# Kernel tuning notes

Hardware: AMD Instinct MI355X
Metric: run time of the kernel (lower is better)

Reference implementation:

```python
import jax, jax.numpy as jnp
import numpy as np

NUM_HEADS = 16
EMBED_DIM = 1024
HEAD_DIM = EMBED_DIM // NUM_HEADS  # 64


def setup_inputs() -> dict:
    key = jax.random.key(0)
    k1, k2, k3 = jax.random.split(key, 3)
    x = jax.random.normal(k1, (2, 2048, EMBED_DIM), dtype=jnp.float32)
    # torch Linear(head_dim, 3*head_dim): weight [3*hd, hd], bias [3*hd]
    # stored here as W_qkv [hd, 3*hd] so that y = x @ W_qkv + b
    lim = 1.0 / np.sqrt(HEAD_DIM)
    W_qkv = jax.random.uniform(k2, (HEAD_DIM, 3 * HEAD_DIM), minval=-lim, maxval=lim, dtype=jnp.float32)
    b_qkv = jax.random.uniform(k3, (3 * HEAD_DIM,), minval=-lim, maxval=lim, dtype=jnp.float32)
    return {"x": x, "W_qkv": W_qkv, "b_qkv": b_qkv}


def reference(x, W_qkv, b_qkv):
    B, T, E = x.shape
    # [B, T, E] -> [B, H, T, hd]
    xh = x.reshape(B, T, NUM_HEADS, HEAD_DIM).transpose(0, 2, 1, 3)
    qkv = xh @ W_qkv + b_qkv  # [B, H, T, 3*hd], shared weights across heads
    q, k, v = jnp.split(qkv, 3, axis=-1)
    scale = 1.0 / jnp.sqrt(jnp.asarray(HEAD_DIM, dtype=x.dtype))
    scores = jnp.einsum('bhqd,bhkd->bhqk', q, k) * scale  # [B, H, T, T]
    attn = jax.nn.softmax(scores, axis=-1)
    out = jnp.einsum('bhqk,bhkd->bhqd', attn, v)  # [B, H, T, hd]
    return out.transpose(0, 2, 1, 3).reshape(B, T, E)
```

## Files before the change

kernel.cpp:

```cpp
#include <hip/hip_runtime.h>
#include <hip/hip_bf16.h>

#define T_SEQ   2048
#define EMBED   1024
#define HD      64
#define NHEADS  16
#define NBH     32
#define QSCALE  0.18033688011112042f

typedef __attribute__((ext_vector_type(8))) short short8;
typedef __attribute__((ext_vector_type(4))) float f32x4;
typedef __attribute__((ext_vector_type(2))) unsigned int uint2v;

#if __has_builtin(__builtin_amdgcn_exp2f)
#define EXP2F __builtin_amdgcn_exp2f
#else
#define EXP2F exp2f
#endif

__device__ __forceinline__ ushort bf16r(float f) {
  union { float f; unsigned u; } v; v.f = f;
  return (ushort)((v.u + 0x8000u) >> 16);
}

__device__ __forceinline__ unsigned pk2bf(float a, float b) {
  union { float f; unsigned u; } ua, ub; ua.f = a; ub.f = b;
  return __builtin_amdgcn_perm(ub.u + 0x8000u, ua.u + 0x8000u, 0x07060302u);
}

__device__ __forceinline__ void async16(const ushort* g, ushort* l) {
  __builtin_amdgcn_global_load_lds(
      (const __attribute__((address_space(1))) unsigned int*)g,
      (__attribute__((address_space(3))) unsigned int*)l, 16, 0, 0);
}

__global__ __launch_bounds__(256) void prep_w(const float* __restrict__ W,
                                              ushort* __restrict__ Wg) {
  const int i = blockIdx.x * 256 + threadIdx.x;
  const int d = i / 192, c = i - d * 192;
  const int phys = c * 64 + (((d >> 3) ^ (c & 7)) << 3) + (d & 7);
  Wg[phys] = bf16r(W[i]);
}

__global__ __launch_bounds__(256) void qkv_proj(
    const float* __restrict__ x, const ushort* __restrict__ Wg,
    const float* __restrict__ bias,
    ushort* __restrict__ Qws, ushort* __restrict__ Kws,
    ushort* __restrict__ Vtws) {
  __shared__ ushort WtL[192 * 64];
  __shared__ float bl[192];

  const int bx = blockIdx.x;
  const int b  = bx >> 9;
  const int h  = (bx >> 5) & 15;
  const int t0 = (bx & 31) * 64;
  const int tid = threadIdx.x;
  const int wave = tid >> 6, lane = tid & 63;
  const int quad = lane >> 4, n16 = lane & 15;

  const int trow = t0 + wave * 16 + n16;
  const float* xr = x + ((size_t)(b * T_SEQ + trow)) * EMBED + h * HD;
  short8 xa[2];
#pragma unroll
  for (int ks = 0; ks < 2; ks++) {
    f32x4 v0 = *(const f32x4*)(xr + ks * 32 + quad * 8);
    f32x4 v1 = *(const f32x4*)(xr + ks * 32 + quad * 8 + 4);
    short8 f;
    ((unsigned*)&f)[0] = pk2bf(v0[0], v0[1]);
    ((unsigned*)&f)[1] = pk2bf(v0[2], v0[3]);
    ((unsigned*)&f)[2] = pk2bf(v1[0], v1[1]);
    ((unsigned*)&f)[3] = pk2bf(v1[2], v1[3]);
    xa[ks] = f;
  }

#pragma unroll
  for (int it = 0; it < 6; it++)
    async16(Wg + it * 2048 + tid * 8, WtL + it * 2048 + wave * 512);
  if (tid < 192) bl[tid] = bias[tid];
  __syncthreads();

  const int bh = b * NHEADS + h;
  const size_t qkbase = (size_t)bh * T_SEQ * HD;
  const int tw = t0 + wave * 16;
  const int sw = n16 & 7;

#pragma unroll
  for (int nt = 0; nt < 12; nt++) {
    const ushort* wrow = WtL + (nt * 16 + n16) * 64;
    const short8 wb0 = *(short8*)(wrow + ((quad ^ sw) << 3));
    const short8 wb1 = *(short8*)(wrow + (((4 | quad) ^ sw) << 3));
    const float bv = bl[nt * 16 + n16];
    f32x4 acc = (f32x4){0.f, 0.f, 0.f, 0.f};
    acc = __builtin_amdgcn_mfma_f32_16x16x32_bf16(xa[0], wb0, acc, 0, 0, 0);
    acc = __builtin_amdgcn_mfma_f32_16x16x32_bf16(xa[1], wb1, acc, 0, 0, 0);
    if (nt < 4) {
      const int d = nt * 16 + n16;
#pragma unroll
      for (int r = 0; r < 4; r++)
        Qws[qkbase + (size_t)(tw + quad * 4 + r) * HD + d] =
            bf16r((acc[r] + bv) * QSCALE);
    } else if (nt < 8) {
      const int d = (nt - 4) * 16 + n16;
#pragma unroll
      for (int r = 0; r < 4; r++)
        Kws[qkbase + (size_t)(tw + quad * 4 + r) * HD + d] =
            bf16r(acc[r] + bv);
    } else {
      const int d = (nt - 8) * 16 + n16;
      const int tcol = tw + quad * 4;
      uint2v pk;
      pk.x = pk2bf(acc[0] + bv, acc[1] + bv);
      pk.y = pk2bf(acc[2] + bv, acc[3] + bv);
      *(uint2v*)(Vtws + (size_t)(bh * HD + d) * T_SEQ + tcol) = pk;
    }
  }
}

__global__ __launch_bounds__(256) void flash_attn(
    const ushort* __restrict__ Qws, const ushort* __restrict__ Kws,
    const ushort* __restrict__ Vtws, float* __restrict__ out) {
  __shared__ ushort Ks[2][64 * 64];
  __shared__ ushort Vs[2][64 * 64];
  __shared__ ushort Ps[4 * 32 * 72];

  const int bx = blockIdx.x;
  const int bh = bx >> 4;
  const int q0 = (bx & 15) * 128;
  const int b = bh >> 4, h = bh & 15;
  const int tid = threadIdx.x;
  const int wave = tid >> 6, lane = tid & 63;
  const int quad = lane >> 4, n16 = lane & 15;

  const ushort* Qb = Qws + (size_t)bh * T_SEQ * HD;
  const ushort* Kb = Kws + (size_t)bh * T_SEQ * HD;
  const ushort* Vb = Vtws + (size_t)bh * HD * T_SEQ;

  short8 qa[2][2];
#pragma unroll
  for (int mt = 0; mt < 2; mt++)
#pragma unroll
    for (int ks = 0; ks < 2; ks++) {
      const int row = q0 + wave * 32 + mt * 16 + n16;
      qa[mt][ks] = *(const short8*)(Qb + (size_t)row * HD + ks * 32 + quad * 8);
    }

  const int sr = tid >> 3, sp = tid & 7;
  const int sl = (sp ^ (sr & 7)) * 8;
  const ushort* srcK0 = Kb + (size_t)sr * HD + sl;
  const ushort* srcK1 = Kb + (size_t)(sr + 32) * HD + sl;
  const ushort* srcV0 = Vb + (size_t)sr * T_SEQ + sl;
  const ushort* srcV1 = Vb + (size_t)(sr + 32) * T_SEQ + sl;

  int foff[4][2];
#pragma unroll
  for (int nt = 0; nt < 4; nt++)
#pragma unroll
    for (int ks = 0; ks < 2; ks++)
      foff[nt][ks] = (nt * 16 + n16) * 64 + ((((ks << 2) | quad) ^ (n16 & 7)) << 3);

  f32x4 o[2][4];
  float lsum[2] = {0.f, 0.f};
#pragma unroll
  for (int mt = 0; mt < 2; mt++)
#pragma unroll
    for (int nt = 0; nt < 4; nt++) o[mt][nt] = (f32x4){0.f, 0.f, 0.f, 0.f};

  ushort* Pw = Ps + wave * 32 * 72;

  async16(srcK0, Ks[0] + wave * 512);
  async16(srcK1, Ks[0] + 2048 + wave * 512);
  async16(srcV0, Vs[0] + wave * 512);
  async16(srcV1, Vs[0] + 2048 + wave * 512);
  __syncthreads();

  for (int kt = 0; kt < 32; kt++) {
    const int bsel = kt & 1;
    if (kt < 31) {
      const size_t kK = (size_t)(kt + 1) * 64 * HD;
      const size_t kV = (size_t)(kt + 1) * 64;
      async16(srcK0 + kK, Ks[bsel ^ 1] + wave * 512);
      async16(srcK1 + kK, Ks[bsel ^ 1] + 2048 + wave * 512);
      async16(srcV0 + kV, Vs[bsel ^ 1] + wave * 512);
      async16(srcV1 + kV, Vs[bsel ^ 1] + 2048 + wave * 512);
    }
    const ushort* Kt = Ks[bsel];
    const ushort* Vt = Vs[bsel];

    f32x4 s[2][4];
#pragma unroll
    for (int nt = 0; nt < 4; nt++) {
      const short8 ka0 = *(short8*)(Kt + foff[nt][0]);
      const short8 ka1 = *(short8*)(Kt + foff[nt][1]);
#pragma unroll
      for (int mt = 0; mt < 2; mt++) {
        f32x4 acc = (f32x4){0.f, 0.f, 0.f, 0.f};
        acc = __builtin_amdgcn_mfma_f32_16x16x32_bf16(ka0, qa[mt][0], acc, 0, 0, 0);
        acc = __builtin_amdgcn_mfma_f32_16x16x32_bf16(ka1, qa[mt][1], acc, 0, 0, 0);
        s[mt][nt] = acc;
      }
    }

#pragma unroll
    for (int mt = 0; mt < 2; mt++) {
#pragma unroll
      for (int nt = 0; nt < 4; nt++) {
        float p0 = EXP2F(s[mt][nt][0]), p1 = EXP2F(s[mt][nt][1]);
        float p2 = EXP2F(s[mt][nt][2]), p3 = EXP2F(s[mt][nt][3]);
        lsum[mt] += (p0 + p1) + (p2 + p3);
        uint2v pk;
        pk.x = pk2bf(p0, p1);
        pk.y = pk2bf(p2, p3);
        *(uint2v*)(Pw + (mt * 16 + n16) * 72 + nt * 16 + quad * 4) = pk;
      }
    }

    short8 pa[2][2];
#pragma unroll
    for (int mt = 0; mt < 2; mt++)
#pragma unroll
      for (int ks = 0; ks < 2; ks++)
        pa[mt][ks] = *(short8*)(Pw + (mt * 16 + n16) * 72 + ks * 32 + quad * 8);
#pragma unroll
    for (int nt = 0; nt < 4; nt++) {
      const short8 vb0 = *(short8*)(Vt + foff[nt][0]);
      const short8 vb1 = *(short8*)(Vt + foff[nt][1]);
#pragma unroll
      for (int mt = 0; mt < 2; mt++) {
        o[mt][nt] = __builtin_amdgcn_mfma_f32_16x16x32_bf16(pa[mt][0], vb0, o[mt][nt], 0, 0, 0);
        o[mt][nt] = __builtin_amdgcn_mfma_f32_16x16x32_bf16(pa[mt][1], vb1, o[mt][nt], 0, 0, 0);
      }
    }
    __syncthreads();
  }

#pragma unroll
  for (int mt = 0; mt < 2; mt++) {
    lsum[mt] += __shfl_xor(lsum[mt], 16, 64);
    lsum[mt] += __shfl_xor(lsum[mt], 32, 64);
  }
  float* Lw = (float*)Pw;
  if (lane < 16) { Lw[n16] = lsum[0]; Lw[16 + n16] = lsum[1]; }

#pragma unroll
  for (int mt = 0; mt < 2; mt++) {
#pragma unroll
    for (int r = 0; r < 4; r++) {
      const int row = q0 + wave * 32 + mt * 16 + quad * 4 + r;
      const float rl = 1.0f / Lw[mt * 16 + quad * 4 + r];
#pragma unroll
      for (int nt = 0; nt < 4; nt++) {
        const int d = nt * 16 + n16;
        out[(size_t)(b * T_SEQ + row) * EMBED + h * HD + d] = o[mt][nt][r] * rl;
      }
    }
  }
}

extern "C" void kernel_launch(void* const* d_in, const int* in_sizes, int n_in,
                              void* d_out, int out_size, void* d_ws, size_t ws_size,
                              hipStream_t stream) {
  (void)in_sizes; (void)n_in; (void)out_size; (void)ws_size;
  const float* x    = (const float*)d_in[0];
  const float* W    = (const float*)d_in[1];
  const float* bias = (const float*)d_in[2];
  float* out = (float*)d_out;

  const size_t elems = (size_t)NBH * T_SEQ * HD;
  ushort* Qws  = (ushort*)d_ws;
  ushort* Kws  = Qws + elems;
  ushort* Vtws = Kws + elems;
  ushort* Wg   = Vtws + elems;

  prep_w<<<dim3(48), dim3(256), 0, stream>>>(W, Wg);
  qkv_proj<<<dim3(1024), dim3(256), 0, stream>>>(x, Wg, bias, Qws, Kws, Vtws);
  flash_attn<<<dim3(512), dim3(256), 0, stream>>>(Qws, Kws, Vtws, out);
}
```

Baseline: 136.6 us.

## Keep P in registers via transposed PV MFMA, drop LDS round-trip

The attention kernel now computes O^T = V^T·P^T with 16x16x16 bf16 MFMAs. The exponentiated score fragments therefore feed the second matmul directly from registers instead of being written to and re-read from a shared-memory P buffer. The output layout changes to row-per-lane, so the row sums need no LDS exchange and the stores become 16-byte vector writes. Float-to-bf16 packing also switches to the hardware cvt_pk instruction when it is available. The cost is twice as many MFMA instructions of half the K depth, plus smaller 8-byte V fragment reads from LDS.

Measured after the change: 139.9 us. 1.02x slower.

```diff
diff --git a/kernel.cpp b/kernel.cpp
--- a/kernel.cpp
+++ b/kernel.cpp
@@ -9,6 +9,7 @@
 #define QSCALE  0.18033688011112042f
 
 typedef __attribute__((ext_vector_type(8))) short short8;
+typedef __attribute__((ext_vector_type(4))) short s16x4;
 typedef __attribute__((ext_vector_type(4))) float f32x4;
 typedef __attribute__((ext_vector_type(2))) unsigned int uint2v;
 
@@ -23,10 +24,32 @@
   return (ushort)((v.u + 0x8000u) >> 16);
 }
 
-__device__ __forceinline__ unsigned pk2bf(float a, float b) {
+__device__ __forceinline__ unsigned pk2bf_perm(float a, float b) {
   union { float f; unsigned u; } ua, ub; ua.f = a; ub.f = b;
   return __builtin_amdgcn_perm(ub.u + 0x8000u, ua.u + 0x8000u, 0x07060302u);
 }
+#if __has_builtin(__builtin_amdgcn_cvt_pk_bf16_f32)
+typedef __attribute__((ext_vector_type(2))) __bf16 bf16x2;
+__device__ __forceinline__ unsigned pkbf(float a, float b) {
+  union { bf16x2 v; unsigned u; } c;
+  c.v = __builtin_amdgcn_cvt_pk_bf16_f32(a, b);
+  return c.u;
+}
+#else
+#define pkbf pk2bf_perm
+#endif
+
+#if __has_builtin(__builtin_amdgcn_mfma_f32_16x16x16bf16_1k)
+__device__ __forceinline__ f32x4 MFMA16(s16x4 A, s16x4 B, f32x4 C) {
+  return __builtin_amdgcn_mfma_f32_16x16x16bf16_1k(A, B, C, 0, 0, 0);
+}
+#else
+__device__ __forceinline__ f32x4 MFMA16(s16x4 A, s16x4 B, f32x4 C) {
+  short8 a8 = (short8){A[0], A[1], A[2], A[3], 0, 0, 0, 0};
+  short8 b8 = (short8){B[0], B[1], B[2], B[3], 0, 0, 0, 0};
+  return __builtin_amdgcn_mfma_f32_16x16x32_bf16(a8, b8, C, 0, 0, 0);
+}
+#endif
 
 __device__ __forceinline__ void async16(const ushort* g, ushort* l) {
   __builtin_amdgcn_global_load_lds(
@@ -66,10 +89,10 @@
     f32x4 v0 = *(const f32x4*)(xr + ks * 32 + quad * 8);
     f32x4 v1 = *(const f32x4*)(xr + ks * 32 + quad * 8 + 4);
     short8 f;
-    ((unsigned*)&f)[0] = pk2bf(v0[0], v0[1]);
-    ((unsigned*)&f)[1] = pk2bf(v0[2], v0[3]);
-    ((unsigned*)&f)[2] = pk2bf(v1[0], v1[1]);
-    ((unsigned*)&f)[3] = pk2bf(v1[2], v1[3]);
+    ((unsigned*)&f)[0] = pkbf(v0[0], v0[1]);
+    ((unsigned*)&f)[1] = pkbf(v0[2], v0[3]);
+    ((unsigned*)&f)[2] = pkbf(v1[0], v1[1]);
+    ((unsigned*)&f)[3] = pkbf(v1[2], v1[3]);
     xa[ks] = f;
   }
 
@@ -109,8 +132,8 @@
       const int d = (nt - 8) * 16 + n16;
       const int tcol = tw + quad * 4;
       uint2v pk;
-      pk.x = pk2bf(acc[0] + bv, acc[1] + bv);
-      pk.y = pk2bf(acc[2] + bv, acc[3] + bv);
+      pk.x = pkbf(acc[0] + bv, acc[1] + bv);
+      pk.y = pkbf(acc[2] + bv, acc[3] + bv);
       *(uint2v*)(Vtws + (size_t)(bh * HD + d) * T_SEQ + tcol) = pk;
     }
   }
@@ -121,7 +144,6 @@
     const ushort* __restrict__ Vtws, float* __restrict__ out) {
   __shared__ ushort Ks[2][64 * 64];
   __shared__ ushort Vs[2][64 * 64];
-  __shared__ ushort Ps[4 * 32 * 72];
 
   const int bx = blockIdx.x;
   const int bh = bx >> 4;
@@ -151,21 +173,22 @@
   const ushort* srcV0 = Vb + (size_t)sr * T_SEQ + sl;
   const ushort* srcV1 = Vb + (size_t)(sr + 32) * T_SEQ + sl;
 
-  int foff[4][2];
+  int koff[2];
+#pragma unroll
+  for (int ks = 0; ks < 2; ks++)
+    koff[ks] = n16 * 64 + ((((ks << 2) | quad) ^ (n16 & 7)) << 3);
+  int voff[4];
 #pragma unroll
   for (int nt = 0; nt < 4; nt++)
-#pragma unroll
-    for (int ks = 0; ks < 2; ks++)
-      foff[nt][ks] = (nt * 16 + n16) * 64 + ((((ks << 2) | quad) ^ (n16 & 7)) << 3);
+    voff[nt] = n16 * 64 + ((((nt << 1) | (quad >> 1)) ^ (n16 & 7)) << 3) +
+               ((quad & 1) << 2);
 
   f32x4 o[2][4];
   float lsum[2] = {0.f, 0.f};
 #pragma unroll
   for (int mt = 0; mt < 2; mt++)
 #pragma unroll
-    for (int nt = 0; nt < 4; nt++) o[mt][nt] = (f32x4){0.f, 0.f, 0.f, 0.f};
-
-  ushort* Pw = Ps + wave * 32 * 72;
+    for (int db = 0; db < 4; db++) o[mt][db] = (f32x4){0.f, 0.f, 0.f, 0.f};
 
   async16(srcK0, Ks[0] + wave * 512);
   async16(srcK1, Ks[0] + 2048 + wave * 512);
@@ -189,8 +212,8 @@
     f32x4 s[2][4];
 #pragma unroll
     for (int nt = 0; nt < 4; nt++) {
-      const short8 ka0 = *(short8*)(Kt + foff[nt][0]);
-      const short8 ka1 = *(short8*)(Kt + foff[nt][1]);
+      const short8 ka0 = *(short8*)(Kt + (nt << 10) + koff[0]);
+      const short8 ka1 = *(short8*)(Kt + (nt << 10) + koff[1]);
 #pragma unroll
       for (int mt = 0; mt < 2; mt++) {
         f32x4 acc = (f32x4){0.f, 0.f, 0.f, 0.f};
@@ -200,6 +223,7 @@
       }
     }
 
+    s16x4 pb[2][4];
 #pragma unroll
     for (int mt = 0; mt < 2; mt++) {
 #pragma unroll
@@ -207,28 +231,24 @@
         float p0 = EXP2F(s[mt][nt][0]), p1 = EXP2F(s[mt][nt][1]);
         float p2 = EXP2F(s[mt][nt][2]), p3 = EXP2F(s[mt][nt][3]);
         lsum[mt] += (p0 + p1) + (p2 + p3);
-        uint2v pk;
-        pk.x = pk2bf(p0, p1);
-        pk.y = pk2bf(p2, p3);
-        *(uint2v*)(Pw + (mt * 16 + n16) * 72 + nt * 16 + quad * 4) = pk;
+        s16x4 pv;
+        ((unsigned*)&pv)[0] = pkbf(p0, p1);
+        ((unsigned*)&pv)[1] = pkbf(p2, p3);
+        pb[mt][nt] = pv;
       }
     }
 
-    short8 pa[2][2];
-#pragma unroll
-    for (int mt = 0; mt < 2; mt++)
-#pragma unroll
-      for (int ks = 0; ks < 2; ks++)
-        pa[mt][ks] = *(short8*)(Pw + (mt * 16 + n16) * 72 + ks * 32 + quad * 8);
-#pragma unroll
-    for (int nt = 0; nt < 4; nt++) {
-      const short8 vb0 = *(short8*)(Vt + foff[nt][0]);
-      const short8 vb1 = *(short8*)(Vt + foff[nt][1]);
-#pragma unroll
-      for (int mt = 0; mt < 2; mt++) {
-        o[mt][nt] = __builtin_amdgcn_mfma_f32_16x16x32_bf16(pa[mt][0], vb0, o[mt][nt], 0, 0, 0);
-        o[mt][nt] = __builtin_amdgcn_mfma_f32_16x16x32_bf16(pa[mt][1], vb1, o[mt][nt], 0, 0, 0);
-      }
+#pragma unroll
+    for (int db = 0; db < 4; db++) {
+      s16x4 va[4];
+#pragma unroll
+      for (int nt = 0; nt < 4; nt++)
+        va[nt] = *(s16x4*)(Vt + (db << 10) + voff[nt]);
+#pragma unroll
+      for (int mt = 0; mt < 2; mt++)
+#pragma unroll
+        for (int nt = 0; nt < 4; nt++)
+          o[mt][db] = MFMA16(va[nt], pb[mt][nt], o[mt][db]);
     }
     __syncthreads();
   }
@@ -237,22 +257,12 @@
   for (int mt = 0; mt < 2; mt++) {
     lsum[mt] += __shfl_xor(lsum[mt], 16, 64);
     lsum[mt] += __shfl_xor(lsum[mt], 32, 64);
-  }
-  float* Lw = (float*)Pw;
-  if (lane < 16) { Lw[n16] = lsum[0]; Lw[16 + n16] = lsum[1]; }
-
-#pragma unroll
-  for (int mt = 0; mt < 2; mt++) {
-#pragma unroll
-    for (int r = 0; r < 4; r++) {
-      const int row = q0 + wave * 32 + mt * 16 + quad * 4 + r;
-      const float rl = 1.0f / Lw[mt * 16 + quad * 4 + r];
-#pragma unroll
-      for (int nt = 0; nt < 4; nt++) {
-        const int d = nt * 16 + n16;
-        out[(size_t)(b * T_SEQ + row) * EMBED + h * HD + d] = o[mt][nt][r] * rl;
-      }
-    }
+    const float rl = 1.0f / lsum[mt];
+    const int row = q0 + wave * 32 + mt * 16 + n16;
+    float* op = out + (size_t)(b * T_SEQ + row) * EMBED + h * HD + quad * 4;
+#pragma unroll
+    for (int db = 0; db < 4; db++)
+      *(f32x4*)(op + db * 16) = o[mt][db] * rl;
   }
 }
 
```
